# Optimization experiments

Hardware: AMD Instinct MI355X
Metric: run time of the kernel (lower is better)

## Reference

```python
import jax, jax.numpy as jnp
import numpy as np

B, N, C, H = 1024, 49, 1024, 32      # windows, window_area (7*7), dim, heads
HD = C // H                          # 32 head dim
HDL = max(1, int(HD * 0.25))         # 8 lite head dim
LD = HDL * H                         # 256 lite dim
TAB = (2 * 7 - 1) ** 2               # 169 rel-pos table rows
SCALE = HD ** -0.5
SCALE_L = HDL ** -0.5


def setup_inputs() -> dict:
    key = jax.random.key(0)
    ks = jax.random.split(key, 13)
    f = lambda i, shape, s=0.02: jax.random.normal(ks[i], shape, jnp.float32) * s
    return {
        "x": jax.random.normal(ks[0], (B, N, C), jnp.float32),
        "qkv_w": f(1, (C, 3 * C)),           # stored (in, out): y = x @ W + b
        "qkv_b": jnp.zeros((3 * C,), jnp.float32),
        "rpb_table": f(2, (TAB, H)),
        "rel_idx": jax.random.randint(ks[3], (N, N), 0, TAB, dtype=jnp.int32),
        "proj_w": f(4, (C, C)),
        "proj_b": jnp.zeros((C,), jnp.float32),
        "ql_w": f(5, (C, LD)),
        "kl_w": f(6, (C, LD)),
        "vl_w": f(7, (C, LD)),
        "dp_w": f(8, (LD, C), 1e-4),         # diff_proj init std=1e-4
        "dp_b": jnp.zeros((C,), jnp.float32),
        "diff_gamma": jnp.float32(0.02),
        "lam1_raw": jnp.float32(-2.0),
        "lam2_raw": jnp.float32(-2.0),
    }


def _forward(x, qkv_w, qkv_b, rpb_table, proj_w, proj_b,
             ql_w, kl_w, vl_w, dp_w, dp_b,
             diff_gamma, lam1_raw, lam2_raw, rel_idx):
    b, n, c = x.shape
    # qkv projection -> (3, B, H, N, HD)
    qkv = (x @ qkv_w + qkv_b).reshape(b, n, 3, H, HD).transpose(2, 0, 3, 1, 4)
    q, k, v = qkv[0], qkv[1], qkv[2]
    # relative position bias gather -> (1, H, N, N)
    bias = rpb_table[rel_idx.reshape(-1)].reshape(n, n, H).transpose(2, 0, 1)[None]
    attn = jnp.einsum("bhqd,bhkd->bhqk", q * SCALE, k) + bias
    attn_soft = jax.nn.softmax(attn, axis=-1)
    x_out = jnp.einsum("bhqk,bhkd->bhqd", attn_soft, v)
    x_out = x_out.transpose(0, 2, 1, 3).reshape(b, n, c)
    # differential lite branch (dim == 1024 -> use_diff)
    q_l = (x @ ql_w).reshape(b, n, H, HDL).transpose(0, 2, 1, 3)
    k_l = (x @ kl_w).reshape(b, n, H, HDL).transpose(0, 2, 1, 3)
    v_l = (x @ vl_w).reshape(b, n, H, HDL).transpose(0, 2, 1, 3)
    attn_l = jnp.einsum("bhqd,bhkd->bhqk", q_l * SCALE_L, k_l) + bias
    lam1 = jax.nn.sigmoid(lam1_raw)
    lam2 = jax.nn.sigmoid(lam2_raw)
    diff = lam1 * jax.nn.softmax(attn_l, axis=-1) - lam2 * jax.lax.stop_gradient(attn_soft)
    delta_v = jnp.einsum("bhqk,bhkd->bhqd", diff, v_l).transpose(0, 2, 1, 3).reshape(b, n, LD)
    x_out = x_out + diff_gamma * (delta_v @ dp_w + dp_b)
    return x_out @ proj_w + proj_b


def reference(x, qkv_w, qkv_b, rpb_table, rel_idx, proj_w, proj_b,
              ql_w, kl_w, vl_w, dp_w, dp_b, diff_gamma, lam1_raw, lam2_raw):
    return _forward(x, qkv_w, qkv_b, rpb_table, proj_w, proj_b,
                    ql_w, kl_w, vl_w, dp_w, dp_b,
                    diff_gamma, lam1_raw, lam2_raw, rel_idx)
```

## Files before the change

### kernel.cpp

```cpp
#include <hip/hip_runtime.h>
#include <cstdint>
#include <cstddef>

typedef __bf16 bf16_t;
typedef float f32x4 __attribute__((ext_vector_type(4)));
typedef __bf16 bf16x8 __attribute__((ext_vector_type(8)));

#define GLOAD_LDS16(gp, lp)                                                        \
    __builtin_amdgcn_global_load_lds(                                              \
        (const __attribute__((address_space(1))) void*)(gp),                       \
        (__attribute__((address_space(3))) void*)(lp), 16, 0, 0)

template <typename OutT>
__global__ __launch_bounds__(256, 2)
void gemm_bt(const bf16_t* __restrict__ A, const bf16_t* __restrict__ BT,
             OutT* __restrict__ C, const float* __restrict__ bias,
             int M, int K, int ldA, int ldBT, int ldC)
{
    __shared__ __align__(16) bf16_t As[2][8192];
    __shared__ __align__(16) bf16_t Bs[2][8192];

    const int bn0 = blockIdx.x * 128;
    const int bm0 = blockIdx.y * 128;
    const int tid  = threadIdx.x;
    const int lane = tid & 63;
    const int w    = tid >> 6;
    const int wr   = w >> 1, wc = w & 1;
    const int lm   = lane & 15, lq = lane >> 4;

    f32x4 acc[4][4];
    #pragma unroll
    for (int i = 0; i < 4; i++)
        #pragma unroll
        for (int j = 0; j < 4; j++) acc[i][j] = (f32x4){0.f, 0.f, 0.f, 0.f};

    const bf16_t* aptr[4];
    const bf16_t* bptr[4];
    #pragma unroll
    for (int ci = 0; ci < 4; ci++) {
        const int c    = w * 4 + ci;
        const int ks   = c >> 3, tile = c & 7;
        const int col  = ks * 32 + lq * 8;
        int arow = bm0 + tile * 16 + lm;
        if (arow > M - 1) arow = M - 1;
        aptr[ci] = A  + (size_t)arow * ldA + col;
        bptr[ci] = BT + (size_t)(bn0 + tile * 16 + lm) * ldBT + col;
    }

    const int nt = K >> 6;

    #pragma unroll
    for (int ci = 0; ci < 4; ci++) {
        const int c = w * 4 + ci;
        GLOAD_LDS16(aptr[ci], &As[0][c * 512]);
        GLOAD_LDS16(bptr[ci], &Bs[0][c * 512]);
    }
    __syncthreads();

    for (int t = 0; t < nt; ++t) {
        const int cur = t & 1;
        if (t + 1 < nt) {
            const int k0 = (t + 1) << 6;
            #pragma unroll
            for (int ci = 0; ci < 4; ci++) {
                const int c = w * 4 + ci;
                GLOAD_LDS16(aptr[ci] + k0, &As[cur ^ 1][c * 512]);
                GLOAD_LDS16(bptr[ci] + k0, &Bs[cur ^ 1][c * 512]);
            }
        }
        #pragma unroll
        for (int ks = 0; ks < 2; ks++) {
            bf16x8 af[4], bfr[4];
            #pragma unroll
            for (int t4 = 0; t4 < 4; t4++) {
                af[t4]  = *(const bf16x8*)&As[cur][(ks * 8 + wr * 4 + t4) * 512 + lane * 8];
                bfr[t4] = *(const bf16x8*)&Bs[cur][(ks * 8 + wc * 4 + t4) * 512 + lane * 8];
            }
            #pragma unroll
            for (int mt = 0; mt < 4; mt++)
                #pragma unroll
                for (int nt2 = 0; nt2 < 4; nt2++)
                    acc[mt][nt2] = __builtin_amdgcn_mfma_f32_16x16x32_bf16(
                        af[mt], bfr[nt2], acc[mt][nt2], 0, 0, 0);
        }
        __syncthreads();
    }

    float bv[4];
    #pragma unroll
    for (int nt2 = 0; nt2 < 4; nt2++)
        bv[nt2] = bias ? bias[bn0 + wc * 64 + nt2 * 16 + lm] : 0.f;
    #pragma unroll
    for (int mt = 0; mt < 4; mt++)
        #pragma unroll
        for (int r2 = 0; r2 < 4; r2++) {
            const int row = bm0 + wr * 64 + mt * 16 + lq * 4 + r2;
            if (row >= M) continue;
            OutT* cp = C + (size_t)row * ldC + bn0 + wc * 64 + lm;
            #pragma unroll
            for (int nt2 = 0; nt2 < 4; nt2++)
                cp[nt2 * 16] = (OutT)(acc[mt][nt2][r2] + bv[nt2]);
        }
}

template <typename SrcT>
__global__ void transpose_to_bf16(const SrcT* __restrict__ src, bf16_t* __restrict__ dst,
                                  int K, int N, int ldsrc, int lddst,
                                  const float* __restrict__ scale_ptr)
{
    __shared__ float tile[32][33];
    const int k0 = blockIdx.x * 32, n0 = blockIdx.y * 32;
    const int tx = threadIdx.x & 31, ty = threadIdx.x >> 5;
    #pragma unroll
    for (int i = 0; i < 4; i++) {
        int k = k0 + ty + 8 * i;
        tile[ty + 8 * i][tx] = (k < K && n0 + tx < N)
            ? (float)src[(size_t)k * ldsrc + n0 + tx] : 0.f;
    }
    __syncthreads();
    const float s = scale_ptr ? *scale_ptr : 1.0f;
    #pragma unroll
    for (int i = 0; i < 4; i++) {
        int n = n0 + ty + 8 * i, k = k0 + tx;
        if (n < N && k < K)
            dst[(size_t)n * lddst + k] = (bf16_t)(s * tile[tx][ty + 8 * i]);
    }
}

__global__ void cast_f32_bf16(const float* __restrict__ src, bf16_t* __restrict__ dst, long n)
{
    long i = ((long)blockIdx.x * blockDim.x + threadIdx.x) * 4;
    if (i >= n) return;
    const float4 v = *(const float4*)(src + i);
    bf16_t d0 = (bf16_t)v.x, d1 = (bf16_t)v.y, d2 = (bf16_t)v.z, d3 = (bf16_t)v.w;
    dst[i] = d0; dst[i + 1] = d1; dst[i + 2] = d2; dst[i + 3] = d3;
}

__global__ void prep_biasA(const float* __restrict__ qkv_b, float* __restrict__ biasA) {
    int n = blockIdx.x * 256 + threadIdx.x;
    if (n < 3840) biasA[n] = (n < 3072) ? qkv_b[n] : 0.f;
}

__global__ void prep_biasO(const float* __restrict__ proj_b, const float* __restrict__ dp_b,
                           const float* __restrict__ proj_w, const float* __restrict__ dgamma,
                           float* __restrict__ biasO) {
    int n = blockIdx.x * 256 + threadIdx.x;
    if (n >= 1024) return;
    float acc = 0.f;
    for (int m = 0; m < 1024; m++) acc += dp_b[m] * proj_w[m * 1024 + n];
    biasO[n] = proj_b[n] + (*dgamma) * acc;
}

__global__ void prep_biasH(const float* __restrict__ rpb, const int* __restrict__ rel,
                           float* __restrict__ biasH) {
    int t = blockIdx.x * 256 + threadIdx.x;
    if (t >= 32 * 49 * 49) return;
    int h = t & 31, ij = t >> 5;
    biasH[(size_t)h * 2401 + ij] = rpb[(size_t)rel[ij] * 32 + h];
}

__global__ __launch_bounds__(64)
void attn_kernel(const bf16_t* __restrict__ QKVL, const float* __restrict__ biasH,
                 bf16_t* __restrict__ AD,
                 const float* __restrict__ lam1p, const float* __restrict__ lam2p)
{
    constexpr float SCALE   = 0.17677669529663687f;
    constexpr float SCALE_L = 0.35355339059327373f;
    const int h  = blockIdx.x & 31;
    const int wb = blockIdx.x >> 5;
    const int lane = threadIdx.x;
    __shared__ float Ks[49][32];
    __shared__ float Vs[49][32];
    __shared__ float KLs[49][8];
    __shared__ float VLs[49][8];
    const size_t base = (size_t)wb * 49 * 3840;

    for (int idx = lane; idx < 196; idx += 64) {
        const int r = idx >> 2, s = idx & 3;
        const bf16x8 kv = *(const bf16x8*)(QKVL + base + (size_t)r * 3840 + 1024 + h * 32 + s * 8);
        const bf16x8 vv = *(const bf16x8*)(QKVL + base + (size_t)r * 3840 + 2048 + h * 32 + s * 8);
        #pragma unroll
        for (int e = 0; e < 8; e++) { Ks[r][s * 8 + e] = (float)kv[e]; Vs[r][s * 8 + e] = (float)vv[e]; }
    }
    for (int r = lane; r < 49; r += 64) {
        const bf16x8 kl = *(const bf16x8*)(QKVL + base + (size_t)r * 3840 + 3328 + h * 8);
        const bf16x8 vl = *(const bf16x8*)(QKVL + base + (size_t)r * 3840 + 3584 + h * 8);
        #pragma unroll
        for (int e = 0; e < 8; e++) { KLs[r][e] = (float)kl[e]; VLs[r][e] = (float)vl[e]; }
    }
    __syncthreads();
    const int i = lane;
    if (i >= 49) return;

    float q[32], qlv[8];
    const bf16_t* qp = QKVL + base + (size_t)i * 3840 + h * 32;
    #pragma unroll
    for (int s = 0; s < 4; s++) {
        const bf16x8 t = *(const bf16x8*)(qp + s * 8);
        #pragma unroll
        for (int e = 0; e < 8; e++) q[s * 8 + e] = (float)t[e] * SCALE;
    }
    {
        const bf16x8 t = *(const bf16x8*)(QKVL + base + (size_t)i * 3840 + 3072 + h * 8);
        #pragma unroll
        for (int e = 0; e < 8; e++) qlv[e] = (float)t[e] * SCALE_L;
    }
    const float* bias = biasH + ((size_t)h * 49 + i) * 49;

    float lg[49], lgl[49];
    #pragma unroll
    for (int j = 0; j < 49; j++) {
        float d = 0.f;
        #pragma unroll
        for (int dd = 0; dd < 32; dd++) d += q[dd] * Ks[j][dd];
        lg[j] = d + bias[j];
    }
    #pragma unroll
    for (int j = 0; j < 49; j++) {
        float d = 0.f;
        #pragma unroll
        for (int dd = 0; dd < 8; dd++) d += qlv[dd] * KLs[j][dd];
        lgl[j] = d + bias[j];
    }
    float m1 = -1e30f, m2 = -1e30f;
    #pragma unroll
    for (int j = 0; j < 49; j++) { m1 = fmaxf(m1, lg[j]); m2 = fmaxf(m2, lgl[j]); }
    float s1 = 0.f, s2 = 0.f;
    #pragma unroll
    for (int j = 0; j < 49; j++) {
        lg[j]  = __expf(lg[j]  - m1); s1 += lg[j];
        lgl[j] = __expf(lgl[j] - m2); s2 += lgl[j];
    }
    const float r1 = 1.f / s1, r2 = 1.f / s2;
    const float l1 = 1.f / (1.f + __expf(-*lam1p));
    const float l2 = 1.f / (1.f + __expf(-*lam2p));

    float o[32], ov[8];
    #pragma unroll
    for (int dd = 0; dd < 32; dd++) o[dd] = 0.f;
    #pragma unroll
    for (int dd = 0; dd < 8; dd++) ov[dd] = 0.f;
    #pragma unroll
    for (int j = 0; j < 49; j++) {
        const float a  = lg[j] * r1;
        const float df = l1 * (lgl[j] * r2) - l2 * a;
        #pragma unroll
        for (int dd = 0; dd < 32; dd++) o[dd] += a * Vs[j][dd];
        #pragma unroll
        for (int dd = 0; dd < 8; dd++)  ov[dd] += df * VLs[j][dd];
    }
    bf16_t* orow = AD + ((size_t)wb * 49 + i) * 1280;
    #pragma unroll
    for (int s = 0; s < 4; s++) {
        bf16x8 t;
        #pragma unroll
        for (int e = 0; e < 8; e++) t[e] = (bf16_t)o[s * 8 + e];
        *(bf16x8*)(orow + h * 32 + s * 8) = t;
    }
    {
        bf16x8 t;
        #pragma unroll
        for (int e = 0; e < 8; e++) t[e] = (bf16_t)ov[e];
        *(bf16x8*)(orow + 1024 + h * 8) = t;
    }
}

extern "C" void kernel_launch(void* const* d_in, const int* in_sizes, int n_in,
                              void* d_out, int out_size, void* d_ws, size_t ws_size,
                              hipStream_t stream)
{
    const float* x      = (const float*)d_in[0];
    const float* qkv_w  = (const float*)d_in[1];
    const float* qkv_b  = (const float*)d_in[2];
    const float* rpb    = (const float*)d_in[3];
    const int*   rel    = (const int*)d_in[4];
    const float* proj_w = (const float*)d_in[5];
    const float* proj_b = (const float*)d_in[6];
    const float* ql_w   = (const float*)d_in[7];
    const float* kl_w   = (const float*)d_in[8];
    const float* vl_w   = (const float*)d_in[9];
    const float* dp_w   = (const float*)d_in[10];
    const float* dp_b   = (const float*)d_in[11];
    const float* dgamma = (const float*)d_in[12];
    const float* lam1   = (const float*)d_in[13];
    const float* lam2   = (const float*)d_in[14];
    float* out = (float*)d_out;
    (void)in_sizes; (void)n_in; (void)out_size;

    char* p = (char*)d_ws;
    auto alloc = [&](size_t bytes) { char* r = p; p += (bytes + 255) & ~(size_t)255; return r; };
    bf16_t* W1T   = (bf16_t*)alloc((size_t)3840 * 1024 * 2);
    bf16_t* W2T   = (bf16_t*)alloc((size_t)1024 * 1280 * 2);
    bf16_t* DPb   = (bf16_t*)alloc((size_t)256 * 1024 * 2);
    bf16_t* Ptmp  = (bf16_t*)alloc((size_t)256 * 1024 * 2);
    float*  biasA = (float*) alloc(3840 * 4);
    float*  biasO = (float*) alloc(1024 * 4);
    float*  biasH = (float*) alloc((size_t)32 * 2401 * 4);
    const size_t fixed = (size_t)(p - (char*)d_ws);
    int CB = 1024;
    while (CB > 1 && fixed + (size_t)CB * 49 * 6144 * 2 + 1024 > ws_size) CB >>= 1;
    bf16_t* Xb   = (bf16_t*)alloc((size_t)CB * 49 * 1024 * 2);
    bf16_t* QKVL = (bf16_t*)alloc((size_t)CB * 49 * 3840 * 2);
    bf16_t* AD   = (bf16_t*)alloc((size_t)CB * 49 * 1280 * 2);

    transpose_to_bf16<float><<<dim3(32, 96), 256, 0, stream>>>(qkv_w, W1T,                     1024, 3072, 3072, 1024, nullptr);
    transpose_to_bf16<float><<<dim3(32, 8),  256, 0, stream>>>(ql_w,  W1T + (size_t)3072*1024, 1024, 256,  256,  1024, nullptr);
    transpose_to_bf16<float><<<dim3(32, 8),  256, 0, stream>>>(kl_w,  W1T + (size_t)3328*1024, 1024, 256,  256,  1024, nullptr);
    transpose_to_bf16<float><<<dim3(32, 8),  256, 0, stream>>>(vl_w,  W1T + (size_t)3584*1024, 1024, 256,  256,  1024, nullptr);
    transpose_to_bf16<float><<<dim3(32, 32), 256, 0, stream>>>(proj_w, W2T,                    1024, 1024, 1024, 1280, nullptr);
    cast_f32_bf16<<<dim3((256 * 1024 / 4 + 255) / 256), 256, 0, stream>>>(dp_w, DPb, 256 * 1024);
    gemm_bt<bf16_t><<<dim3(8, 2), 256, 0, stream>>>(DPb, W2T, Ptmp, nullptr, 256, 1024, 1024, 1280, 1024);
    transpose_to_bf16<bf16_t><<<dim3(8, 32), 256, 0, stream>>>(Ptmp, W2T + 1024, 256, 1024, 1024, 1280, dgamma);
    prep_biasA<<<dim3(15), 256, 0, stream>>>(qkv_b, biasA);
    prep_biasO<<<dim3(4),  256, 0, stream>>>(proj_b, dp_b, proj_w, dgamma, biasO);
    prep_biasH<<<dim3((32 * 2401 + 255) / 256), 256, 0, stream>>>(rpb, rel, biasH);

    const int nchunk = 1024 / CB;
    const int Mc = CB * 49;
    const int gy = (Mc + 127) / 128;
    for (int cc = 0; cc < nchunk; cc++) {
        const float* xc = x + (size_t)cc * Mc * 1024;
        cast_f32_bf16<<<dim3(((long)Mc * 1024 / 4 + 255) / 256), 256, 0, stream>>>(xc, Xb, (long)Mc * 1024);
        gemm_bt<bf16_t><<<dim3(3840 / 128, gy), 256, 0, stream>>>(
            Xb, W1T, QKVL, biasA, Mc, 1024, 1024, 1024, 3840);
        attn_kernel<<<dim3(CB * 32), 64, 0, stream>>>(QKVL, biasH, AD, lam1, lam2);
        gemm_bt<float><<<dim3(1024 / 128, gy), 256, 0, stream>>>(
            AD, W2T, out + (size_t)cc * Mc * 1024, biasO, Mc, 1280, 1280, 1280, 1024);
    }
}
```

Measured before the change: 2.018 ms.

## Enlarge GEMM tiles to 256x256 with 8 waves and a barrier-split prefetch pipeline

The bf16 GEMM moves from 128x128 tiles with 4 waves to 256x256 tiles with 8 waves, each wave computing a 128x64 sub-tile. This raises arithmetic intensity per LDS load and cuts global traffic. The K loop now keeps two stages in flight: it issues the load two iterations ahead, uses explicit vmcnt waits and raw s_barrier instead of __syncthreads, and raises wave priority around the MFMA block. The biasO precompute is split across 64 blocks using atomicAdd. The larger tile uses 128 KB of LDS and more accumulator registers, which may limit occupancy. It also leaves fewer blocks in the grid, for example only 4 column blocks in the output GEMM.

```diff
diff --git a/kernel.cpp b/kernel.cpp
--- a/kernel.cpp
+++ b/kernel.cpp
@@ -12,25 +12,25 @@
         (__attribute__((address_space(3))) void*)(lp), 16, 0, 0)
 
 template <typename OutT>
-__global__ __launch_bounds__(256, 2)
+__global__ __launch_bounds__(512, 2)
 void gemm_bt(const bf16_t* __restrict__ A, const bf16_t* __restrict__ BT,
              OutT* __restrict__ C, const float* __restrict__ bias,
              int M, int K, int ldA, int ldBT, int ldC)
 {
-    __shared__ __align__(16) bf16_t As[2][8192];
-    __shared__ __align__(16) bf16_t Bs[2][8192];
-
-    const int bn0 = blockIdx.x * 128;
-    const int bm0 = blockIdx.y * 128;
+    __shared__ __align__(16) bf16_t As[2][16384];
+    __shared__ __align__(16) bf16_t Bs[2][16384];
+
+    const int bn0 = blockIdx.x * 256;
+    const int bm0 = blockIdx.y * 256;
     const int tid  = threadIdx.x;
     const int lane = tid & 63;
     const int w    = tid >> 6;
-    const int wr   = w >> 1, wc = w & 1;
+    const int wr   = w >> 2, wc = w & 3;
     const int lm   = lane & 15, lq = lane >> 4;
 
-    f32x4 acc[4][4];
-    #pragma unroll
-    for (int i = 0; i < 4; i++)
+    f32x4 acc[8][4];
+    #pragma unroll
+    for (int i = 0; i < 8; i++)
         #pragma unroll
         for (int j = 0; j < 4; j++) acc[i][j] = (f32x4){0.f, 0.f, 0.f, 0.f};
 
@@ -39,7 +39,7 @@
     #pragma unroll
     for (int ci = 0; ci < 4; ci++) {
         const int c    = w * 4 + ci;
-        const int ks   = c >> 3, tile = c & 7;
+        const int ks   = c >> 4, tile = c & 15;
         const int col  = ks * 32 + lq * 8;
         int arow = bm0 + tile * 16 + lm;
         if (arow > M - 1) arow = M - 1;
@@ -49,52 +49,70 @@
 
     const int nt = K >> 6;
 
-    #pragma unroll
-    for (int ci = 0; ci < 4; ci++) {
-        const int c = w * 4 + ci;
-        GLOAD_LDS16(aptr[ci], &As[0][c * 512]);
-        GLOAD_LDS16(bptr[ci], &Bs[0][c * 512]);
-    }
-    __syncthreads();
+#define STAGE(tt, buf)                                                   \
+    {                                                                    \
+        const int k0s = (tt) << 6;                                       \
+        _Pragma("unroll")                                                \
+        for (int ci = 0; ci < 4; ci++) {                                 \
+            const int c = w * 4 + ci;                                    \
+            GLOAD_LDS16(aptr[ci] + k0s, &As[buf][c * 512]);              \
+            GLOAD_LDS16(bptr[ci] + k0s, &Bs[buf][c * 512]);              \
+        }                                                                \
+    }
+
+    STAGE(0, 0);
+    if (nt > 1) {
+        STAGE(1, 1);
+        asm volatile("s_waitcnt vmcnt(8)" ::: "memory");
+    } else {
+        asm volatile("s_waitcnt vmcnt(0)" ::: "memory");
+    }
+    __builtin_amdgcn_s_barrier();
+    __builtin_amdgcn_sched_barrier(0);
 
     for (int t = 0; t < nt; ++t) {
         const int cur = t & 1;
-        if (t + 1 < nt) {
-            const int k0 = (t + 1) << 6;
+        #pragma unroll
+        for (int ks = 0; ks < 2; ks++) {
+            bf16x8 af[8], bfv[4];
             #pragma unroll
-            for (int ci = 0; ci < 4; ci++) {
-                const int c = w * 4 + ci;
-                GLOAD_LDS16(aptr[ci] + k0, &As[cur ^ 1][c * 512]);
-                GLOAD_LDS16(bptr[ci] + k0, &Bs[cur ^ 1][c * 512]);
-            }
-        }
-        #pragma unroll
-        for (int ks = 0; ks < 2; ks++) {
-            bf16x8 af[4], bfr[4];
+            for (int t4 = 0; t4 < 8; t4++)
+                af[t4] = *(const bf16x8*)&As[cur][(ks * 16 + wr * 8 + t4) * 512 + lane * 8];
             #pragma unroll
-            for (int t4 = 0; t4 < 4; t4++) {
-                af[t4]  = *(const bf16x8*)&As[cur][(ks * 8 + wr * 4 + t4) * 512 + lane * 8];
-                bfr[t4] = *(const bf16x8*)&Bs[cur][(ks * 8 + wc * 4 + t4) * 512 + lane * 8];
-            }
+            for (int t4 = 0; t4 < 4; t4++)
+                bfv[t4] = *(const bf16x8*)&Bs[cur][(ks * 16 + wc * 4 + t4) * 512 + lane * 8];
+            __builtin_amdgcn_s_setprio(1);
             #pragma unroll
-            for (int mt = 0; mt < 4; mt++)
+            for (int mt = 0; mt < 8; mt++)
                 #pragma unroll
                 for (int nt2 = 0; nt2 < 4; nt2++)
                     acc[mt][nt2] = __builtin_amdgcn_mfma_f32_16x16x32_bf16(
-                        af[mt], bfr[nt2], acc[mt][nt2], 0, 0, 0);
+                        af[mt], bfv[nt2], acc[mt][nt2], 0, 0, 0);
+            __builtin_amdgcn_s_setprio(0);
         }
-        __syncthreads();
-    }
+        if (t + 1 < nt) {
+            __builtin_amdgcn_s_barrier();
+            if (t + 2 < nt) {
+                STAGE(t + 2, cur);
+                asm volatile("s_waitcnt vmcnt(8)" ::: "memory");
+            } else {
+                asm volatile("s_waitcnt vmcnt(0)" ::: "memory");
+            }
+            __builtin_amdgcn_s_barrier();
+            __builtin_amdgcn_sched_barrier(0);
+        }
+    }
+#undef STAGE
 
     float bv[4];
     #pragma unroll
     for (int nt2 = 0; nt2 < 4; nt2++)
         bv[nt2] = bias ? bias[bn0 + wc * 64 + nt2 * 16 + lm] : 0.f;
     #pragma unroll
-    for (int mt = 0; mt < 4; mt++)
+    for (int mt = 0; mt < 8; mt++)
         #pragma unroll
         for (int r2 = 0; r2 < 4; r2++) {
-            const int row = bm0 + wr * 64 + mt * 16 + lq * 4 + r2;
+            const int row = bm0 + wr * 128 + mt * 16 + lq * 4 + r2;
             if (row >= M) continue;
             OutT* cp = C + (size_t)row * ldC + bn0 + wc * 64 + lm;
             #pragma unroll
@@ -141,14 +159,21 @@
     if (n < 3840) biasA[n] = (n < 3072) ? qkv_b[n] : 0.f;
 }
 
-__global__ void prep_biasO(const float* __restrict__ proj_b, const float* __restrict__ dp_b,
-                           const float* __restrict__ proj_w, const float* __restrict__ dgamma,
-                           float* __restrict__ biasO) {
+__global__ void prep_biasO_init(const float* __restrict__ proj_b, float* __restrict__ biasO) {
     int n = blockIdx.x * 256 + threadIdx.x;
-    if (n >= 1024) return;
+    if (n < 1024) biasO[n] = proj_b[n];
+}
+
+__global__ void prep_biasO_acc(const float* __restrict__ dp_b,
+                               const float* __restrict__ proj_w,
+                               const float* __restrict__ dgamma,
+                               float* __restrict__ biasO) {
+    const int n  = blockIdx.x * 256 + threadIdx.x;
+    const int m0 = blockIdx.y * 64;
     float acc = 0.f;
-    for (int m = 0; m < 1024; m++) acc += dp_b[m] * proj_w[m * 1024 + n];
-    biasO[n] = proj_b[n] + (*dgamma) * acc;
+    #pragma unroll 8
+    for (int m = m0; m < m0 + 64; m++) acc += dp_b[m] * proj_w[m * 1024 + n];
+    atomicAdd(biasO + n, (*dgamma) * acc);
 }
 
 __global__ void prep_biasH(const float* __restrict__ rpb, const int* __restrict__ rel,
@@ -309,22 +334,23 @@
     transpose_to_bf16<float><<<dim3(32, 8),  256, 0, stream>>>(vl_w,  W1T + (size_t)3584*1024, 1024, 256,  256,  1024, nullptr);
     transpose_to_bf16<float><<<dim3(32, 32), 256, 0, stream>>>(proj_w, W2T,                    1024, 1024, 1024, 1280, nullptr);
     cast_f32_bf16<<<dim3((256 * 1024 / 4 + 255) / 256), 256, 0, stream>>>(dp_w, DPb, 256 * 1024);
-    gemm_bt<bf16_t><<<dim3(8, 2), 256, 0, stream>>>(DPb, W2T, Ptmp, nullptr, 256, 1024, 1024, 1280, 1024);
+    gemm_bt<bf16_t><<<dim3(4, 1), 512, 0, stream>>>(DPb, W2T, Ptmp, nullptr, 256, 1024, 1024, 1280, 1024);
     transpose_to_bf16<bf16_t><<<dim3(8, 32), 256, 0, stream>>>(Ptmp, W2T + 1024, 256, 1024, 1024, 1280, dgamma);
     prep_biasA<<<dim3(15), 256, 0, stream>>>(qkv_b, biasA);
-    prep_biasO<<<dim3(4),  256, 0, stream>>>(proj_b, dp_b, proj_w, dgamma, biasO);
+    prep_biasO_init<<<dim3(4), 256, 0, stream>>>(proj_b, biasO);
+    prep_biasO_acc<<<dim3(4, 16), 256, 0, stream>>>(dp_b, proj_w, dgamma, biasO);
     prep_biasH<<<dim3((32 * 2401 + 255) / 256), 256, 0, stream>>>(rpb, rel, biasH);
 
     const int nchunk = 1024 / CB;
     const int Mc = CB * 49;
-    const int gy = (Mc + 127) / 128;
+    const int gy = (Mc + 255) / 256;
     for (int cc = 0; cc < nchunk; cc++) {
         const float* xc = x + (size_t)cc * Mc * 1024;
         cast_f32_bf16<<<dim3(((long)Mc * 1024 / 4 + 255) / 256), 256, 0, stream>>>(xc, Xb, (long)Mc * 1024);
-        gemm_bt<bf16_t><<<dim3(3840 / 128, gy), 256, 0, stream>>>(
+        gemm_bt<bf16_t><<<dim3(3840 / 256, gy), 512, 0, stream>>>(
             Xb, W1T, QKVL, biasA, Mc, 1024, 1024, 1024, 3840);
         attn_kernel<<<dim3(CB * 32), 64, 0, stream>>>(QKVL, biasH, AD, lam1, lam2);
-        gemm_bt<float><<<dim3(1024 / 128, gy), 256, 0, stream>>>(
+        gemm_bt<float><<<dim3(1024 / 256, gy), 512, 0, stream>>>(
             AD, W2T, out + (size_t)cc * Mc * 1024, biasO, Mc, 1280, 1280, 1280, 1024);
     }
 }
```

Result: faster. 1.823 ms (-9.7%).
